# Performance work log

Measured on AMD Instinct MI355X. Metric: run time of the kernel, lower is better.

Reference implementation:

```python
import jax, jax.numpy as jnp
import numpy as np

B, S, D = 1, 2048, 2048
NH, NKV = 32, 8
HD = D // NH  # 64
ROPE_THETA = 10000.0


def setup_inputs() -> dict:
    key = jax.random.key(0)
    k1, k2, k3 = jax.random.split(key, 3)
    x = jax.random.normal(k1, (B, S, D), dtype=jnp.float32)
    # real RoPE frequencies (freqs_cis = exp(i * t * theta^(-2j/hd)))
    inv_freq = 1.0 / (ROPE_THETA ** (np.arange(0, HD, 2, dtype=np.float32) / HD))
    t = np.arange(S, dtype=np.float32)
    ang = np.outer(t, inv_freq)  # [S, HD/2]
    cos = jnp.asarray(np.cos(ang), dtype=jnp.float32)
    sin = jnp.asarray(np.sin(ang), dtype=jnp.float32)
    wqkv = jax.random.normal(k2, (NH * HD + 2 * NKV * HD, D), dtype=jnp.float32) * (D ** -0.5)
    wo = jax.random.normal(k3, (D, NH * HD), dtype=jnp.float32) * (D ** -0.5)
    return {"x": x, "cos": cos, "sin": sin, "wqkv": wqkv, "wo": wo}


def _rope(t, cos, sin):
    # t: [b, h, s, hd]; pairs are interleaved (even=real, odd=imag)
    tr = t[..., 0::2]
    ti = t[..., 1::2]
    c = cos[None, None]  # [1,1,s,hd/2]
    s_ = sin[None, None]
    orr = tr * c - ti * s_
    oi = tr * s_ + ti * c
    out = jnp.stack([orr, oi], axis=-1)  # [b,h,s,hd/2,2]
    return out.reshape(t.shape)


def reference(x, cos, sin, wqkv, wo):
    bsz, seqlen, d_model = x.shape
    qkv = jnp.einsum('bsd,ed->bse', x, wqkv)  # fused QKV proj
    q, k, v = jnp.split(qkv, [NH * HD, NH * HD + NKV * HD], axis=-1)
    q = q.reshape(bsz, seqlen, NH, HD).transpose(0, 2, 1, 3)
    k = k.reshape(bsz, seqlen, NKV, HD).transpose(0, 2, 1, 3)
    v = v.reshape(bsz, seqlen, NKV, HD).transpose(0, 2, 1, 3)
    q = _rope(q, cos, sin)
    k = _rope(k, cos, sin)
    # GQA: repeat_interleave kv heads
    rep = NH // NKV
    k_r = jnp.broadcast_to(k[:, :, None], (bsz, NKV, rep, seqlen, HD)).reshape(bsz, NH, seqlen, HD)
    v_r = jnp.broadcast_to(v[:, :, None], (bsz, NKV, rep, seqlen, HD)).reshape(bsz, NH, seqlen, HD)
    scale = 1.0 / jnp.sqrt(jnp.asarray(HD, dtype=x.dtype))
    scores = jnp.einsum('bhqd,bhkd->bhqk', q, k_r) * scale
    causal = jnp.tril(jnp.ones((seqlen, seqlen), dtype=bool))
    scores = jnp.where(causal[None, None], scores, jnp.asarray(-jnp.inf, dtype=scores.dtype))
    attn = jax.nn.softmax(scores, axis=-1)
    y = jnp.einsum('bhqk,bhkd->bhqd', attn, v_r)
    y = y.transpose(0, 2, 1, 3).reshape(bsz, seqlen, NH * HD)
    y = jnp.einsum('bse,de->bsd', y, wo)
    return y
```

## Files before the change

### kernel.cpp

```cpp
#include <hip/hip_runtime.h>
#include <hip/hip_bf16.h>

typedef __attribute__((ext_vector_type(8))) short bf16x8;
typedef __attribute__((ext_vector_type(4))) float f32x4;
typedef __attribute__((ext_vector_type(16))) float f32x16;
typedef __attribute__((ext_vector_type(2))) unsigned int u32x2;

#define S_LEN 2048
#define DMODEL 2048
#define NHEAD 32
#define NKVH 8
#define HDIM 64
#define EQKV 3072

#if defined(__has_builtin)
#if __has_builtin(__builtin_amdgcn_global_load_lds)
#define HAVE_GLL 1
#endif
#endif

__device__ __forceinline__ unsigned short f2bf(float f) {
  unsigned int u = __float_as_uint(f);
  u = (u + 0x7FFFu + ((u >> 16) & 1u)) >> 16;
  return (unsigned short)u;
}

__device__ __forceinline__ f32x4 mfma16(bf16x8 a, bf16x8 b, f32x4 c) {
  return __builtin_amdgcn_mfma_f32_16x16x32_bf16(a, b, c, 0, 0, 0);
}
__device__ __forceinline__ f32x16 mfma32(bf16x8 a, bf16x8 b, f32x16 c) {
  return __builtin_amdgcn_mfma_f32_32x32x16_bf16(a, b, c, 0, 0, 0);
}

__device__ __forceinline__ unsigned cvtpk(float a, float b) {
  unsigned r;
  asm("v_cvt_pk_bf16_f32 %0, %1, %2" : "=v"(r) : "v"(a), "v"(b));
  return r;
}

__device__ __forceinline__ void plswap(unsigned& a, unsigned& b) {
  u32x2 r = __builtin_amdgcn_permlane32_swap(a, b, false, false);
  a = r.x;
  b = r.y;
}
__device__ __forceinline__ void plswapf(float& a, float& b) {
  unsigned ua = __float_as_uint(a), ub = __float_as_uint(b);
  plswap(ua, ub);
  a = __uint_as_float(ua);
  b = __uint_as_float(ub);
}

#if HAVE_GLL
__device__ __forceinline__ void gload16(const unsigned short* g,
                                        unsigned short* l) {
  __builtin_amdgcn_global_load_lds(
      (const __attribute__((address_space(1))) unsigned int*)g,
      (__attribute__((address_space(3))) unsigned int*)l, 16, 0, 0);
}
#endif

__global__ void cast3_kernel(const float* __restrict__ x,
                             const float* __restrict__ wqkv,
                             const float* __restrict__ wo,
                             unsigned short* __restrict__ xb,
                             unsigned short* __restrict__ wb,
                             unsigned short* __restrict__ wob) {
  int i = blockIdx.x * blockDim.x + threadIdx.x;
  const float* s;
  unsigned short* d;
  int j;
  if (i < 1048576) {
    s = x; d = xb; j = i;
  } else if (i < 2621440) {
    s = wqkv; d = wb; j = i - 1048576;
  } else {
    s = wo; d = wob; j = i - 2621440;
  }
  float4 v = ((const float4*)s)[j];
  ushort4 o;
  o.x = f2bf(v.x); o.y = f2bf(v.y); o.z = f2bf(v.z); o.w = f2bf(v.w);
  ((ushort4*)d)[j] = o;
}

template <int MODE, int BM>
__launch_bounds__(256)
__global__ void gemm_bt(const unsigned short* __restrict__ A,
                        const unsigned short* __restrict__ B,
                        float* __restrict__ C,
                        unsigned short* __restrict__ VB, int M, int N, int K) {
  constexpr int MF = BM / 32;
  constexpr int AI = BM / 32;
  __shared__ unsigned short As[2][BM * 64];
  __shared__ unsigned short Bs[2][64 * 64];
  const int tid = threadIdx.x;
  const int w = tid >> 6, l = tid & 63;
  const int wr = w >> 1, wc = w & 1;
  const int nwg = gridDim.x * gridDim.y;
  const int bid0 = blockIdx.y * gridDim.x + blockIdx.x;
  const int swz = (bid0 & 7) * (nwg >> 3) + (bid0 >> 3);
  const int bm = swz / gridDim.x, bn = swz % gridDim.x;
  const int lr = l & 15, lq = l >> 4;

  f32x4 acc[MF][2];
#pragma unroll
  for (int m = 0; m < MF; ++m)
#pragma unroll
    for (int n = 0; n < 2; ++n) acc[m][n] = (f32x4)0.f;

  const unsigned short* gA[AI];
  const unsigned short* gB[2];
#pragma unroll
  for (int i = 0; i < AI; ++i) {
    int c = i * 256 + tid;
    int row = c >> 3;
    int sc = (c & 7) ^ (row & 7);
    gA[i] = A + (size_t)(bm * BM + row) * K + sc * 8;
  }
#pragma unroll
  for (int i = 0; i < 2; ++i) {
    int c = i * 256 + tid;
    int row = c >> 3;
    int sc = (c & 7) ^ (row & 7);
    gB[i] = B + (size_t)(bn * 64 + row) * K + sc * 8;
  }

#if HAVE_GLL
#define STAGE(bufi, k0)                                            \
  do {                                                             \
    _Pragma("unroll") for (int i = 0; i < AI; ++i)                 \
        gload16(gA[i] + (k0), &As[bufi][(i * 256 + w * 64) * 8]);  \
    _Pragma("unroll") for (int i = 0; i < 2; ++i)                  \
        gload16(gB[i] + (k0), &Bs[bufi][(i * 256 + w * 64) * 8]);  \
  } while (0)
#else
#define STAGE(bufi, k0)                                            \
  do {                                                             \
    _Pragma("unroll") for (int i = 0; i < AI; ++i) {               \
      int c = i * 256 + tid;                                       \
      *(uint4*)(&As[bufi][c * 8]) = *(const uint4*)(gA[i] + (k0)); \
    }                                                              \
    _Pragma("unroll") for (int i = 0; i < 2; ++i) {                \
      int c = i * 256 + tid;                                       \
      *(uint4*)(&Bs[bufi][c * 8]) = *(const uint4*)(gB[i] + (k0)); \
    }                                                              \
  } while (0)
#endif

#define COMPUTE(bufi)                                                     \
  do {                                                                    \
    _Pragma("unroll") for (int ks = 0; ks < 2; ++ks) {                    \
      bf16x8 af[MF], bfr[2];                                              \
      _Pragma("unroll") for (int m = 0; m < MF; ++m) {                    \
        int row = wr * (BM / 2) + m * 16 + lr;                            \
        int ch = (ks * 4 + lq) ^ (row & 7);                               \
        af[m] = *(const bf16x8*)(&As[bufi][row * 64 + ch * 8]);           \
      }                                                                   \
      _Pragma("unroll") for (int n = 0; n < 2; ++n) {                     \
        int row = wc * 32 + n * 16 + lr;                                  \
        int ch = (ks * 4 + lq) ^ (row & 7);                               \
        bfr[n] = *(const bf16x8*)(&Bs[bufi][row * 64 + ch * 8]);          \
      }                                                                   \
      _Pragma("unroll") for (int m = 0; m < MF; ++m)                      \
          _Pragma("unroll") for (int n = 0; n < 2; ++n)                   \
              acc[m][n] = mfma16(af[m], bfr[n], acc[m][n]);               \
    }                                                                     \
  } while (0)

  const int nt = K >> 6;
  STAGE(0, 0);
  int cur = 0;
#if HAVE_GLL
  for (int t = 0; t < nt - 1; ++t) {
    STAGE(cur ^ 1, (t + 1) * 64);
    if constexpr (BM == 128)
      asm volatile("s_waitcnt vmcnt(6)" ::: "memory");
    else
      asm volatile("s_waitcnt vmcnt(4)" ::: "memory");
    __builtin_amdgcn_sched_barrier(0);
    __builtin_amdgcn_s_barrier();
    COMPUTE(cur);
    asm volatile("s_waitcnt lgkmcnt(0)" ::: "memory");
    __builtin_amdgcn_sched_barrier(0);
    __builtin_amdgcn_s_barrier();
    cur ^= 1;
  }
  asm volatile("s_waitcnt vmcnt(0)" ::: "memory");
  __builtin_amdgcn_sched_barrier(0);
  __builtin_amdgcn_s_barrier();
  COMPUTE(cur);
#else
  for (int t = 0; t < nt; ++t) {
    if (t > 0) STAGE(cur, t * 64);
    __syncthreads();
    COMPUTE(cur);
    __syncthreads();
  }
#endif
#undef STAGE
#undef COMPUTE

  const int r0 = bm * BM + wr * (BM / 2);
  const int c0 = bn * 64 + wc * 32;
  if (MODE == 1 && bn >= 40) {
    const int c0v = c0 - 2560;
#pragma unroll
    for (int m = 0; m < MF; ++m)
#pragma unroll
      for (int n = 0; n < 2; ++n)
#pragma unroll
        for (int r = 0; r < 4; ++r)
          VB[(size_t)(r0 + m * 16 + 4 * lq + r) * 512 + c0v + n * 16 + lr] =
              f2bf(acc[m][n][r]);
  } else {
#pragma unroll
    for (int m = 0; m < MF; ++m)
#pragma unroll
      for (int n = 0; n < 2; ++n)
#pragma unroll
        for (int r = 0; r < 4; ++r)
          C[(size_t)(r0 + m * 16 + 4 * lq + r) * N + c0 + n * 16 + lr] =
              acc[m][n][r];
  }
}

#define KSCALE 0.18033688011112042f
__global__ void rope_vt(const float* __restrict__ qkv,
                        const unsigned short* __restrict__ vb,
                        const float* __restrict__ cosb,
                        const float* __restrict__ sinb,
                        unsigned short* __restrict__ qb,
                        unsigned short* __restrict__ kft,
                        unsigned short* __restrict__ vft) {
  __shared__ unsigned short tile[64][72];
  const int b = blockIdx.x;
  if (b < 2048) {
    const int s = b;
    const float* row = qkv + (size_t)s * EQKV;
    for (int idx = threadIdx.x; idx < 1280; idx += 256) {
      int hh = idx >> 5;
      int m = idx & 31;
      float c = cosb[s * 32 + m];
      float sn = sinb[s * 32 + m];
      if (hh < 32) {
        float tr = row[hh * 64 + 2 * m];
        float ti = row[hh * 64 + 2 * m + 1];
        unsigned int pack = (unsigned int)f2bf(tr * c - ti * sn) |
                            ((unsigned int)f2bf(tr * sn + ti * c) << 16);
        *(unsigned int*)(qb + ((size_t)hh * S_LEN + s) * HDIM + 2 * m) = pack;
      } else {
        int kvh = hh - 32;
        float cs = c * KSCALE, ss = sn * KSCALE;
        float tr = row[2048 + kvh * 64 + 2 * m];
        float ti = row[2048 + kvh * 64 + 2 * m + 1];
        unsigned int pack = (unsigned int)f2bf(tr * cs - ti * ss) |
                            ((unsigned int)f2bf(tr * ss + ti * cs) << 16);
        int kt = s >> 5, lq = s & 31;
        int j = m >> 3, hi = (m >> 2) & 1;
        unsigned short* dst =
            kft +
            ((((size_t)kvh * 64 + kt) * 4 + j) * 64 + lq + 32 * hi) * 8 +
            (m & 3) * 2;
        *(unsigned int*)dst = pack;
      }
    }
  } else {
    const int b2 = b - 2048;
    const int kvh = b2 >> 5;
    const int st = b2 & 31;
    const int t = threadIdx.x;
    {
      const int sl = t >> 2, dg = t & 3;
      const unsigned short* src =
          vb + (size_t)(st * 64 + sl) * 512 + kvh * 64 + dg * 16;
      union U8 { uint4 v; unsigned short e[8]; } a0, a1;
      a0.v = *(const uint4*)src;
      a1.v = *(const uint4*)(src + 8);
#pragma unroll
      for (int j = 0; j < 8; ++j) tile[dg * 16 + j][sl] = a0.e[j];
#pragma unroll
      for (int j = 0; j < 8; ++j) tile[dg * 16 + 8 + j][sl] = a1.e[j];
    }
    __syncthreads();
    {
      const int kt_local = t >> 7, c = (t >> 5) & 3, lq2 = t & 31;
      const int kt = st * 2 + kt_local;
      const int d = ((c >> 1) & 1) * 32 + lq2;
      unsigned short* dbase =
          vft + (((size_t)(kvh * 64 + kt) * 4 + c) * 64) * 8;
#pragma unroll
      for (int hi2 = 0; hi2 < 2; ++hi2) {
        int koff = kt_local * 32 + (c & 1) * 16 + 8 * hi2;
        *(uint4*)(dbase + (lq2 + 32 * hi2) * 8) =
            *(const uint4*)(&tile[d][koff]);
      }
    }
  }
}

__launch_bounds__(256, 3)
__global__ void attn_kernel(const unsigned short* __restrict__ qb,
                            const unsigned short* __restrict__ kft,
                            const unsigned short* __restrict__ vft,
                            unsigned short* __restrict__ aob) {
  __shared__ float buf[4][64][19];
  const int tid = threadIdx.x;
  const int wv = tid >> 6, l = tid & 63;
  const int bid = blockIdx.x;
  const int xcd = bid & 7, idx = bid >> 3;
  const int h = xcd * 4 + (idx & 3);
  const int qt = 63 - (idx >> 2);
  const int kvh = xcd;
  const int q0 = qt << 5;
  const int lq = l & 31;
  const int hi = l >> 5;
  const int qg = q0 + lq;

  const unsigned short* qrow = qb + ((size_t)h * S_LEN + qg) * HDIM + 8 * hi;
  bf16x8 qf[4];
#pragma unroll
  for (int j = 0; j < 4; ++j) qf[j] = *(const bf16x8*)(qrow + 16 * j);

  const unsigned short* kbase = kft + (size_t)kvh * 64 * 2048;
  const unsigned short* vbase = vft + (size_t)kvh * 64 * 2048;

  f32x16 o0 = (f32x16)0.f, o1 = (f32x16)0.f;
  float mrun = -1e30f, lrun = 0.f;
  const int ntile = qt + 1;

  int kt = wv;
  for (; kt + 4 < ntile; kt += 8) {
    const unsigned short* ka = kbase + (size_t)kt * 2048;
    const unsigned short* va = vbase + (size_t)kt * 2048;
    bf16x8 kfa[4], kfb[4], vaa[4], vab[4];
#pragma unroll
    for (int j = 0; j < 4; ++j) {
      kfa[j] = *(const bf16x8*)(ka + 512 * j + l * 8);
      kfb[j] = *(const bf16x8*)(ka + 4 * 2048 + 512 * j + l * 8);
      vaa[j] = *(const bf16x8*)(va + 512 * j + l * 8);
      vab[j] = *(const bf16x8*)(va + 4 * 2048 + 512 * j + l * 8);
    }
    f32x16 sa = (f32x16)0.f, sb = (f32x16)0.f;
    __builtin_amdgcn_s_setprio(1);
#pragma unroll
    for (int j = 0; j < 4; ++j) sa = mfma32(kfa[j], qf[j], sa);
#pragma unroll
    for (int j = 0; j < 4; ++j) sb = mfma32(kfb[j], qf[j], sb);
    __builtin_amdgcn_s_setprio(0);

    float p[32];
#pragma unroll
    for (int r = 0; r < 16; ++r) p[r] = sa[r];
    if (kt + 4 == ntile - 1) {
#pragma unroll
      for (int r = 0; r < 16; ++r) {
        int key = (kt + 4) * 32 + (r & 3) + 8 * (r >> 2) + 4 * hi;
        p[16 + r] = (key > qg) ? -1e30f : sb[r];
      }
    } else {
#pragma unroll
      for (int r = 0; r < 16; ++r) p[16 + r] = sb[r];
    }
    float a0 = fmaxf(fmaxf(p[0], p[1]), p[2]);
    float a1 = fmaxf(fmaxf(p[3], p[4]), p[5]);
    float a2 = fmaxf(fmaxf(p[6], p[7]), p[8]);
    float a3 = fmaxf(fmaxf(p[9], p[10]), p[11]);
    float a4 = fmaxf(fmaxf(p[12], p[13]), p[14]);
    float b0 = fmaxf(fmaxf(p[15], p[16]), p[17]);
    float b1 = fmaxf(fmaxf(p[18], p[19]), p[20]);
    float b2 = fmaxf(fmaxf(p[21], p[22]), p[23]);
    float b3 = fmaxf(fmaxf(p[24], p[25]), p[26]);
    float b4 = fmaxf(fmaxf(p[27], p[28]), p[29]);
    float b5 = fmaxf(p[30], p[31]);
    float mt = fmaxf(fmaxf(fmaxf(fmaxf(a0, a1), fmaxf(a2, a3)),
                           fmaxf(fmaxf(a4, b0), fmaxf(b1, b2))),
                     fmaxf(fmaxf(b3, b4), b5));
    float mto = mt;
    plswapf(mt, mto);
    mt = fmaxf(mt, mto);
    if (!__all(mt - mrun <= 8.f)) {
      float mnew = fmaxf(mrun, mt);
      float al = __builtin_amdgcn_exp2f(mrun - mnew);
      mrun = mnew;
      lrun *= al;
      o0 *= al;
      o1 *= al;
    }
#pragma unroll
    for (int r = 0; r < 32; ++r) p[r] = __builtin_amdgcn_exp2f(p[r] - mrun);
    float s0 = (p[0] + p[1]) + (p[2] + p[3]);
    float s1 = (p[4] + p[5]) + (p[6] + p[7]);
    float s2 = (p[8] + p[9]) + (p[10] + p[11]);
    float s3 = (p[12] + p[13]) + (p[14] + p[15]);
    float s4 = (p[16] + p[17]) + (p[18] + p[19]);
    float s5 = (p[20] + p[21]) + (p[22] + p[23]);
    float s6 = (p[24] + p[25]) + (p[26] + p[27]);
    float s7 = (p[28] + p[29]) + (p[30] + p[31]);
    float ts = ((s0 + s1) + (s2 + s3)) + ((s4 + s5) + (s6 + s7));
    float tso = ts;
    plswapf(ts, tso);
    ts += tso;
    lrun += ts;
    union B8 { unsigned u[4]; bf16x8 v; } pb0a, pb1a, pb0b, pb1b;
    {
      unsigned t0 = cvtpk(p[0], p[1]), t1 = cvtpk(p[4], p[5]);
      plswap(t0, t1);
      pb0a.u[0] = t0; pb0a.u[2] = t1;
    }
    {
      unsigned t0 = cvtpk(p[2], p[3]), t1 = cvtpk(p[6], p[7]);
      plswap(t0, t1);
      pb0a.u[1] = t0; pb0a.u[3] = t1;
    }
    {
      unsigned t0 = cvtpk(p[8], p[9]), t1 = cvtpk(p[12], p[13]);
      plswap(t0, t1);
      pb1a.u[0] = t0; pb1a.u[2] = t1;
    }
    {
      unsigned t0 = cvtpk(p[10], p[11]), t1 = cvtpk(p[14], p[15]);
      plswap(t0, t1);
      pb1a.u[1] = t0; pb1a.u[3] = t1;
    }
    {
      unsigned t0 = cvtpk(p[16], p[17]), t1 = cvtpk(p[20], p[21]);
      plswap(t0, t1);
      pb0b.u[0] = t0; pb0b.u[2] = t1;
    }
    {
      unsigned t0 = cvtpk(p[18], p[19]), t1 = cvtpk(p[22], p[23]);
      plswap(t0, t1);
      pb0b.u[1] = t0; pb0b.u[3] = t1;
    }
    {
      unsigned t0 = cvtpk(p[24], p[25]), t1 = cvtpk(p[28], p[29]);
      plswap(t0, t1);
      pb1b.u[0] = t0; pb1b.u[2] = t1;
    }
    {
      unsigned t0 = cvtpk(p[26], p[27]), t1 = cvtpk(p[30], p[31]);
      plswap(t0, t1);
      pb1b.u[1] = t0; pb1b.u[3] = t1;
    }
    __builtin_amdgcn_s_setprio(1);
    o0 = mfma32(vaa[0], pb0a.v, o0);
    o0 = mfma32(vaa[1], pb1a.v, o0);
    o1 = mfma32(vaa[2], pb0a.v, o1);
    o1 = mfma32(vaa[3], pb1a.v, o1);
    o0 = mfma32(vab[0], pb0b.v, o0);
    o0 = mfma32(vab[1], pb1b.v, o0);
    o1 = mfma32(vab[2], pb0b.v, o1);
    o1 = mfma32(vab[3], pb1b.v, o1);
    __builtin_amdgcn_s_setprio(0);
  }
  if (kt < ntile) {
    const int key0 = kt << 5;
    const unsigned short* kvt = kbase + (size_t)kt * 2048;
    bf16x8 kf0 = *(const bf16x8*)(kvt + l * 8);
    bf16x8 kf1 = *(const bf16x8*)(kvt + 512 + l * 8);
    bf16x8 kf2 = *(const bf16x8*)(kvt + 1024 + l * 8);
    bf16x8 kf3 = *(const bf16x8*)(kvt + 1536 + l * 8);
    const unsigned short* vvt = vbase + (size_t)kt * 2048;
    bf16x8 va00 = *(const bf16x8*)(vvt + l * 8);
    bf16x8 va01 = *(const bf16x8*)(vvt + 512 + l * 8);
    bf16x8 va10 = *(const bf16x8*)(vvt + 1024 + l * 8);
    bf16x8 va11 = *(const bf16x8*)(vvt + 1536 + l * 8);

    f32x16 s = (f32x16)0.f;
    __builtin_amdgcn_s_setprio(1);
    s = mfma32(kf0, qf[0], s);
    s = mfma32(kf1, qf[1], s);
    s = mfma32(kf2, qf[2], s);
    s = mfma32(kf3, qf[3], s);
    __builtin_amdgcn_s_setprio(0);

    float p[16];
    if (kt == ntile - 1) {
#pragma unroll
      for (int r = 0; r < 16; ++r) {
        int key = key0 + (r & 3) + 8 * (r >> 2) + 4 * hi;
        p[r] = (key > qg) ? -1e30f : s[r];
      }
    } else {
#pragma unroll
      for (int r = 0; r < 16; ++r) p[r] = s[r];
    }
    float a0 = fmaxf(fmaxf(p[0], p[1]), p[2]);
    float a1 = fmaxf(fmaxf(p[3], p[4]), p[5]);
    float a2 = fmaxf(fmaxf(p[6], p[7]), p[8]);
    float a3 = fmaxf(fmaxf(p[9], p[10]), p[11]);
    float a4 = fmaxf(fmaxf(p[12], p[13]), p[14]);
    float mt = fmaxf(fmaxf(fmaxf(a0, a1), a2), fmaxf(fmaxf(a3, a4), p[15]));
    float mto = mt;
    plswapf(mt, mto);
    mt = fmaxf(mt, mto);
    if (!__all(mt - mrun <= 8.f)) {
      float mnew = fmaxf(mrun, mt);
      float al = __builtin_amdgcn_exp2f(mrun - mnew);
      mrun = mnew;
      lrun *= al;
      o0 *= al;
      o1 *= al;
    }
#pragma unroll
    for (int r = 0; r < 16; ++r) p[r] = __builtin_amdgcn_exp2f(p[r] - mrun);
    float s0 = (p[0] + p[1]) + (p[2] + p[3]);
    float s1 = (p[4] + p[5]) + (p[6] + p[7]);
    float s2 = (p[8] + p[9]) + (p[10] + p[11]);
    float s3 = (p[12] + p[13]) + (p[14] + p[15]);
    float ts = (s0 + s1) + (s2 + s3);
    float tso = ts;
    plswapf(ts, tso);
    ts += tso;
    lrun += ts;
    union B8 { unsigned u[4]; bf16x8 v; } pb0, pb1;
    {
      unsigned t0 = cvtpk(p[0], p[1]), t1 = cvtpk(p[4], p[5]);
      plswap(t0, t1);
      pb0.u[0] = t0; pb0.u[2] = t1;
    }
    {
      unsigned t0 = cvtpk(p[2], p[3]), t1 = cvtpk(p[6], p[7]);
      plswap(t0, t1);
      pb0.u[1] = t0; pb0.u[3] = t1;
    }
    {
      unsigned t0 = cvtpk(p[8], p[9]), t1 = cvtpk(p[12], p[13]);
      plswap(t0, t1);
      pb1.u[0] = t0; pb1.u[2] = t1;
    }
    {
      unsigned t0 = cvtpk(p[10], p[11]), t1 = cvtpk(p[14], p[15]);
      plswap(t0, t1);
      pb1.u[1] = t0; pb1.u[3] = t1;
    }
    __builtin_amdgcn_s_setprio(1);
    o0 = mfma32(va00, pb0.v, o0);
    o0 = mfma32(va01, pb1.v, o0);
    o1 = mfma32(va10, pb0.v, o1);
    o1 = mfma32(va11, pb1.v, o1);
    __builtin_amdgcn_s_setprio(0);
  }

  {
    union F16 { f32x16 v; f32x4 q[4]; } uu;
    uu.v = o0;
    float* dst = &buf[wv][l][0];
#pragma unroll
    for (int i = 0; i < 4; ++i) *(f32x4*)(dst + 4 * i) = uu.q[i];
    dst[16] = mrun;
    dst[17] = lrun;
  }
  __syncthreads();
  float mfin = -1e30f;
#pragma unroll
  for (int w2 = 0; w2 < 4; ++w2) mfin = fmaxf(mfin, buf[w2][l][16]);
  float lsum = 0.f;
  float scl[4];
#pragma unroll
  for (int w2 = 0; w2 < 4; ++w2) {
    scl[w2] = __builtin_amdgcn_exp2f(buf[w2][l][16] - mfin);
    lsum += buf[w2][l][17] * scl[w2];
  }
  const float inv = 1.f / lsum;
  unsigned short* obase = aob + (size_t)qg * DMODEL + h * 64;
  {
    f32x4 acc = (f32x4)0.f;
#pragma unroll
    for (int w2 = 0; w2 < 4; ++w2)
      acc += *(const f32x4*)&buf[w2][l][wv * 4] * scl[w2];
    unsigned u0 = cvtpk(acc[0] * inv, acc[1] * inv);
    unsigned u1 = cvtpk(acc[2] * inv, acc[3] * inv);
    unsigned short* dsto = obase + 8 * wv + 4 * hi;
    *(unsigned*)(dsto) = u0;
    *(unsigned*)(dsto + 2) = u1;
  }
  __syncthreads();
  {
    union F16 { f32x16 v; f32x4 q[4]; } uu;
    uu.v = o1;
    float* dst = &buf[wv][l][0];
#pragma unroll
    for (int i = 0; i < 4; ++i) *(f32x4*)(dst + 4 * i) = uu.q[i];
  }
  __syncthreads();
  {
    f32x4 acc = (f32x4)0.f;
#pragma unroll
    for (int w2 = 0; w2 < 4; ++w2)
      acc += *(const f32x4*)&buf[w2][l][wv * 4] * scl[w2];
    unsigned u0 = cvtpk(acc[0] * inv, acc[1] * inv);
    unsigned u1 = cvtpk(acc[2] * inv, acc[3] * inv);
    unsigned short* dsto = obase + 32 + 8 * wv + 4 * hi;
    *(unsigned*)(dsto) = u0;
    *(unsigned*)(dsto + 2) = u1;
  }
}

extern "C" void kernel_launch(void* const* d_in, const int* in_sizes, int n_in,
                              void* d_out, int out_size, void* d_ws,
                              size_t ws_size, hipStream_t stream) {
  const float* x = (const float*)d_in[0];
  const float* cosb = (const float*)d_in[1];
  const float* sinb = (const float*)d_in[2];
  const float* wqkv = (const float*)d_in[3];
  const float* wo = (const float*)d_in[4];
  float* out = (float*)d_out;
  char* ws = (char*)d_ws;
  float* qkv = (float*)(ws);
  unsigned short* xb = (unsigned short*)(ws + 25165824);
  unsigned short* wb = (unsigned short*)(ws + 33554432);
  unsigned short* wob = (unsigned short*)(ws + 46137344);
  unsigned short* qb = (unsigned short*)(ws + 54525952);
  unsigned short* kft = (unsigned short*)(ws + 62914560);
  unsigned short* vft = (unsigned short*)(ws + 65011712);
  unsigned short* aob = (unsigned short*)(ws + 67108864);
  unsigned short* vb = (unsigned short*)(ws + 75497472);

  cast3_kernel<<<dim3(3670016 / 256), 256, 0, stream>>>(x, wqkv, wo, xb, wb,
                                                        wob);
  gemm_bt<1, 128><<<dim3(48, 16), 256, 0, stream>>>(xb, wb, qkv, vb, 2048,
                                                    3072, 2048);
  rope_vt<<<dim3(2304), 256, 0, stream>>>(qkv, vb, cosb, sinb, qb, kft, vft);
  attn_kernel<<<dim3(2048), 256, 0, stream>>>(qb, kft, vft, aob);
  gemm_bt<0, 64><<<dim3(32, 32), 256, 0, stream>>>(aob, wob, out, nullptr,
                                                   2048, 2048, 2048);
}
```

Before: 117.1 us.

## Fuse RoPE for Q and K into the QKV GEMM epilogue

Applies the rotary embedding and the K scaling directly in the QKV GEMM epilogue. Adjacent lanes exchange their real and imaginary pair values through a shuffle, and results are written as bf16 straight into the Q layout and the swizzled K layout. The rope kernel shrinks to a V-transpose-only kernel. This removes the fp32 QKV round trip through memory for the Q/K columns and most of one kernel launch, in exchange for scattered 2-byte stores and per-element cos/sin loads in the GEMM epilogue.

```diff
diff --git a/kernel.cpp b/kernel.cpp
--- a/kernel.cpp
+++ b/kernel.cpp
@@ -12,6 +12,7 @@
 #define NKVH 8
 #define HDIM 64
 #define EQKV 3072
+#define KSCALE 0.18033688011112042f
 
 #if defined(__has_builtin)
 #if __has_builtin(__builtin_amdgcn_global_load_lds)
@@ -87,7 +88,12 @@
 __global__ void gemm_bt(const unsigned short* __restrict__ A,
                         const unsigned short* __restrict__ B,
                         float* __restrict__ C,
-                        unsigned short* __restrict__ VB, int M, int N, int K) {
+                        unsigned short* __restrict__ VB,
+                        const float* __restrict__ cosb,
+                        const float* __restrict__ sinb,
+                        unsigned short* __restrict__ qb,
+                        unsigned short* __restrict__ kft,
+                        int M, int N, int K) {
   constexpr int MF = BM / 32;
   constexpr int AI = BM / 32;
   __shared__ unsigned short As[2][BM * 64];
@@ -201,7 +207,37 @@
 
   const int r0 = bm * BM + wr * (BM / 2);
   const int c0 = bn * 64 + wc * 32;
-  if (MODE == 1 && bn >= 40) {
+  if (MODE == 1 && bn < 40) {
+    const bool isK = (bn >= 32);
+#pragma unroll
+    for (int m = 0; m < MF; ++m) {
+#pragma unroll
+      for (int n = 0; n < 2; ++n) {
+        const int d = wc * 32 + n * 16 + lr;
+        const int mp = d >> 1;
+#pragma unroll
+        for (int r = 0; r < 4; ++r) {
+          const int s = r0 + m * 16 + 4 * lq + r;
+          float c = cosb[s * 32 + mp];
+          float sn = sinb[s * 32 + mp];
+          if (isK) { c *= KSCALE; sn *= KSCALE; }
+          float val = acc[m][n][r];
+          float partner = __shfl_xor(val, 1, 64);
+          float out = (lr & 1) ? (partner * sn + val * c)
+                               : (val * c - partner * sn);
+          unsigned short ob = f2bf(out);
+          if (!isK) {
+            qb[((size_t)bn * S_LEN + s) * HDIM + d] = ob;
+          } else {
+            const int kvh = bn - 32;
+            const int kt = s >> 5;
+            kft[((((size_t)kvh * 64 + kt) * 4 + (d >> 4)) * 64 + (s & 31) +
+                 32 * ((d >> 3) & 1)) * 8 + (d & 7)] = ob;
+          }
+        }
+      }
+    }
+  } else if (MODE == 1) {
     const int c0v = c0 - 2560;
 #pragma unroll
     for (int m = 0; m < MF; ++m)
@@ -223,76 +259,36 @@
   }
 }
 
-#define KSCALE 0.18033688011112042f
-__global__ void rope_vt(const float* __restrict__ qkv,
-                        const unsigned short* __restrict__ vb,
-                        const float* __restrict__ cosb,
-                        const float* __restrict__ sinb,
-                        unsigned short* __restrict__ qb,
-                        unsigned short* __restrict__ kft,
-                        unsigned short* __restrict__ vft) {
+__global__ void vt_kernel(const unsigned short* __restrict__ vb,
+                          unsigned short* __restrict__ vft) {
   __shared__ unsigned short tile[64][72];
-  const int b = blockIdx.x;
-  if (b < 2048) {
-    const int s = b;
-    const float* row = qkv + (size_t)s * EQKV;
-    for (int idx = threadIdx.x; idx < 1280; idx += 256) {
-      int hh = idx >> 5;
-      int m = idx & 31;
-      float c = cosb[s * 32 + m];
-      float sn = sinb[s * 32 + m];
-      if (hh < 32) {
-        float tr = row[hh * 64 + 2 * m];
-        float ti = row[hh * 64 + 2 * m + 1];
-        unsigned int pack = (unsigned int)f2bf(tr * c - ti * sn) |
-                            ((unsigned int)f2bf(tr * sn + ti * c) << 16);
-        *(unsigned int*)(qb + ((size_t)hh * S_LEN + s) * HDIM + 2 * m) = pack;
-      } else {
-        int kvh = hh - 32;
-        float cs = c * KSCALE, ss = sn * KSCALE;
-        float tr = row[2048 + kvh * 64 + 2 * m];
-        float ti = row[2048 + kvh * 64 + 2 * m + 1];
-        unsigned int pack = (unsigned int)f2bf(tr * cs - ti * ss) |
-                            ((unsigned int)f2bf(tr * ss + ti * cs) << 16);
-        int kt = s >> 5, lq = s & 31;
-        int j = m >> 3, hi = (m >> 2) & 1;
-        unsigned short* dst =
-            kft +
-            ((((size_t)kvh * 64 + kt) * 4 + j) * 64 + lq + 32 * hi) * 8 +
-            (m & 3) * 2;
-        *(unsigned int*)dst = pack;
-      }
-    }
-  } else {
-    const int b2 = b - 2048;
-    const int kvh = b2 >> 5;
-    const int st = b2 & 31;
-    const int t = threadIdx.x;
-    {
-      const int sl = t >> 2, dg = t & 3;
-      const unsigned short* src =
-          vb + (size_t)(st * 64 + sl) * 512 + kvh * 64 + dg * 16;
-      union U8 { uint4 v; unsigned short e[8]; } a0, a1;
-      a0.v = *(const uint4*)src;
-      a1.v = *(const uint4*)(src + 8);
-#pragma unroll
-      for (int j = 0; j < 8; ++j) tile[dg * 16 + j][sl] = a0.e[j];
-#pragma unroll
-      for (int j = 0; j < 8; ++j) tile[dg * 16 + 8 + j][sl] = a1.e[j];
-    }
-    __syncthreads();
-    {
-      const int kt_local = t >> 7, c = (t >> 5) & 3, lq2 = t & 31;
-      const int kt = st * 2 + kt_local;
-      const int d = ((c >> 1) & 1) * 32 + lq2;
-      unsigned short* dbase =
-          vft + (((size_t)(kvh * 64 + kt) * 4 + c) * 64) * 8;
-#pragma unroll
-      for (int hi2 = 0; hi2 < 2; ++hi2) {
-        int koff = kt_local * 32 + (c & 1) * 16 + 8 * hi2;
-        *(uint4*)(dbase + (lq2 + 32 * hi2) * 8) =
-            *(const uint4*)(&tile[d][koff]);
-      }
+  const int kvh = blockIdx.x >> 5;
+  const int st = blockIdx.x & 31;
+  const int t = threadIdx.x;
+  {
+    const int sl = t >> 2, dg = t & 3;
+    const unsigned short* src =
+        vb + (size_t)(st * 64 + sl) * 512 + kvh * 64 + dg * 16;
+    union U8 { uint4 v; unsigned short e[8]; } a0, a1;
+    a0.v = *(const uint4*)src;
+    a1.v = *(const uint4*)(src + 8);
+#pragma unroll
+    for (int j = 0; j < 8; ++j) tile[dg * 16 + j][sl] = a0.e[j];
+#pragma unroll
+    for (int j = 0; j < 8; ++j) tile[dg * 16 + 8 + j][sl] = a1.e[j];
+  }
+  __syncthreads();
+  {
+    const int kt_local = t >> 7, c = (t >> 5) & 3, lq2 = t & 31;
+    const int kt = st * 2 + kt_local;
+    const int d = ((c >> 1) & 1) * 32 + lq2;
+    unsigned short* dbase =
+        vft + (((size_t)(kvh * 64 + kt) * 4 + c) * 64) * 8;
+#pragma unroll
+    for (int hi2 = 0; hi2 < 2; ++hi2) {
+      int koff = kt_local * 32 + (c & 1) * 16 + 8 * hi2;
+      *(uint4*)(dbase + (lq2 + 32 * hi2) * 8) =
+          *(const uint4*)(&tile[d][koff]);
     }
   }
 }
@@ -618,10 +614,11 @@
 
   cast3_kernel<<<dim3(3670016 / 256), 256, 0, stream>>>(x, wqkv, wo, xb, wb,
                                                         wob);
-  gemm_bt<1, 128><<<dim3(48, 16), 256, 0, stream>>>(xb, wb, qkv, vb, 2048,
-                                                    3072, 2048);
-  rope_vt<<<dim3(2304), 256, 0, stream>>>(qkv, vb, cosb, sinb, qb, kft, vft);
+  gemm_bt<1, 128><<<dim3(48, 16), 256, 0, stream>>>(
+      xb, wb, qkv, vb, cosb, sinb, qb, kft, 2048, 3072, 2048);
+  vt_kernel<<<dim3(256), 256, 0, stream>>>(vb, vft);
   attn_kernel<<<dim3(2048), 256, 0, stream>>>(qb, kft, vft, aob);
-  gemm_bt<0, 64><<<dim3(32, 32), 256, 0, stream>>>(aob, wob, out, nullptr,
-                                                   2048, 2048, 2048);
-}
+  gemm_bt<0, 64><<<dim3(32, 32), 256, 0, stream>>>(
+      aob, wob, out, nullptr, nullptr, nullptr, nullptr, nullptr, 2048, 2048,
+      2048);
+}
```

Measured after the change: 117.5 us. No clear change (+0.4%).
